# Performance work log

Measured on AMD Instinct MI355X. Metric: run time of the kernel, lower is better.

The kernel has to match this reference:

```python
import jax, jax.numpy as jnp
import numpy as np

N = 100000   # nodes
E = 1600000  # edges
F = 128      # num_features
H = 128      # embedding_size
C = 10       # num_classes
G = 64       # graphs in batch


def setup_inputs() -> dict:
    key = jax.random.key(0)
    ks = jax.random.split(key, 10)
    x = jax.random.normal(ks[0], (N, F), jnp.float32)
    edge_index = jax.random.randint(ks[1], (2, E), 0, N)
    batch_index = jnp.sort(jax.random.randint(ks[2], (N,), 0, G))
    glorot = lambda k, shape: jax.random.normal(k, shape, jnp.float32) / np.float32(np.sqrt(shape[0]))
    return {
        "x": x, "edge_index": edge_index, "batch_index": batch_index,
        "W0": glorot(ks[3], (F, H)), "b0": jnp.zeros((H,), jnp.float32),
        "W1": glorot(ks[4], (H, H)), "b1": jnp.zeros((H,), jnp.float32),
        "W2": glorot(ks[5], (H, H)), "b2": jnp.zeros((H,), jnp.float32),
        "W3": glorot(ks[6], (H, H)), "b3": jnp.zeros((H,), jnp.float32),
        "Wout": glorot(ks[7], (2 * H, C)), "bout": jnp.zeros((C,), jnp.float32),
    }


def gcn_conv(x, W, b, src, dst):
    """PyG GCNConv: self-loops + symmetric D^-1/2 (A+I) D^-1/2 normalization."""
    n = x.shape[0]
    # degree with self-loop: deg[i] = 1 + in-degree(i)
    deg = 1.0 + jax.ops.segment_sum(jnp.ones(dst.shape[0], x.dtype), dst, num_segments=n)
    dinv = jax.lax.rsqrt(deg)
    h = x @ W  # [N, H]
    norm = (dinv[src] * dinv[dst])[:, None]  # [E, 1]
    agg = jax.ops.segment_sum(h[src] * norm, dst, num_segments=n)  # scatter-add over edges
    agg = agg + h * (1.0 / deg)[:, None]  # self-loop contribution dinv[i]^2 * h[i]
    return agg + b


def reference(x, edge_index, batch_index, W0, b0, W1, b1, W2, b2, W3, b3, Wout, bout):
    src, dst = edge_index[0], edge_index[1]
    h = jnp.tanh(gcn_conv(x, W0, b0, src, dst))
    h = jnp.tanh(gcn_conv(h, W1, b1, src, dst))
    h = jnp.tanh(gcn_conv(h, W2, b2, src, dst))
    h = jnp.tanh(gcn_conv(h, W3, b3, src, dst))
    # global max pool + global mean pool over batch_index
    gmax = jax.ops.segment_max(h, batch_index, num_segments=G)
    cnt = jax.ops.segment_sum(jnp.ones((h.shape[0],), h.dtype), batch_index, num_segments=G)
    gmean = jax.ops.segment_sum(h, batch_index, num_segments=G) / jnp.maximum(cnt, 1.0)[:, None]
    pooled = jnp.concatenate([gmax, gmean], axis=1)  # [G, 2H]
    out = pooled @ Wout + bout  # [G, C]
    return out, pooled
```

## Files before the change

### kernel.cpp

```cpp
#include <hip/hip_runtime.h>
#include <hip/hip_fp16.h>
#include <cmath>

typedef __attribute__((ext_vector_type(8))) short short8;
typedef __attribute__((ext_vector_type(8))) unsigned short ushort8;
typedef __attribute__((ext_vector_type(8))) _Float16 f16x8;
typedef __attribute__((ext_vector_type(4))) float f32x4;

__device__ __forceinline__ unsigned pk_bf16(float a, float b) {
  unsigned r;
  asm("v_cvt_pk_bf16_f32 %0, %1, %2" : "=v"(r) : "v"(a), "v"(b));
  return r;
}

__device__ __forceinline__ float fast_tanh(float x) {
  float e2 = __expf(2.0f * x);
  return 1.0f - 2.0f * __builtin_amdgcn_rcpf(e2 + 1.0f);
}

#define FM_LO(A, U, W) \
  asm("v_fma_mix_f32 %0, %1, %2, %0 op_sel_hi:[1,0,0]" : "+v"(A) : "v"(U), "v"(W))
#define FM_HI(A, U, W) \
  asm("v_fma_mix_f32 %0, %1, %2, %0 op_sel:[1,0,0] op_sel_hi:[1,0,0]" : "+v"(A) : "v"(U), "v"(W))


__global__ __launch_bounds__(256) void count_wconv(
    const int* __restrict__ dst, int* __restrict__ cnt, int* __restrict__ epos,
    int E, int nc, const float* __restrict__ W0, const float* __restrict__ W1,
    const float* __restrict__ W2, const float* __restrict__ W3,
    unsigned short* __restrict__ Wt0Hi, unsigned short* __restrict__ Wt0Lo,
    unsigned short* __restrict__ WfHi, unsigned short* __restrict__ WfLo) {
  int b = blockIdx.x;
  if (b < nc) {
    int e = b * 256 + threadIdx.x;
    if (e < E) epos[e] = atomicAdd(&cnt[dst[e]], 1);
    return;
  }
  int t = (b - nc) * 256 + threadIdx.x;
  int l = t >> 13;
  int idx = t & 8191;
  const float* W = (l == 0) ? W0 : (l == 1) ? W1 : (l == 2) ? W2 : W3;
  int n = idx & 127, k = (idx >> 7) * 2;
  float w0 = W[k * 128 + n], w1 = W[(k + 1) * 128 + n];
  if (l == 0) {
    unsigned h01 = pk_bf16(w0, w1);
    float hf0 = __uint_as_float(h01 << 16);
    float hf1 = __uint_as_float(h01 & 0xFFFF0000u);
    unsigned l01 = pk_bf16(w0 - hf0, w1 - hf1);
    *(unsigned*)&Wt0Hi[n * 128 + k] = h01;
    *(unsigned*)&Wt0Lo[n * 128 + k] = l01;
  } else {
    __half2 hh = __float22half2_rn(make_float2(w0, w1));
    float r0 = __low2float(hh), r1 = __high2float(hh);
    __half2 ll = __float22half2_rn(make_float2((w0 - r0) * 1024.0f,
                                               (w1 - r1) * 1024.0f));
    *(__half2*)&WfHi[(l - 1) * 16384 + n * 128 + k] = hh;
    *(__half2*)&WfLo[(l - 1) * 16384 + n * 128 + k] = ll;
  }
}


__global__ __launch_bounds__(512) void scan_a(const int* __restrict__ cnt,
                                              int* __restrict__ rs,
                                              int* __restrict__ bsum,
                                              float* __restrict__ dinv,
                                              float* __restrict__ dinv2, int n) {
  __shared__ int s[512];
  int tid = threadIdx.x;
  int gid = blockIdx.x * 512 + tid;
  int v = (gid < n) ? cnt[gid] : 0;
  if (gid < n) {
    float deg = 1.0f + (float)v;
    dinv[gid] = rsqrtf(deg);
    dinv2[gid] = __builtin_amdgcn_rcpf(deg);
  }
  s[tid] = v;
  __syncthreads();
  for (int off = 1; off < 512; off <<= 1) {
    int t = (tid >= off) ? s[tid - off] : 0;
    __syncthreads();
    s[tid] += t;
    __syncthreads();
  }
  if (gid < n) rs[gid] = s[tid] - v;
  if (tid == 511) bsum[blockIdx.x] = s[511];
}

__global__ __launch_bounds__(256) void scan_b(const int* __restrict__ bsum,
                                              int* __restrict__ boff, int nb,
                                              const int* __restrict__ batch,
                                              int* __restrict__ gstart, int n,
                                              int G) {
  __shared__ int s[256];
  int tid = threadIdx.x;
  int v = (tid < nb) ? bsum[tid] : 0;
  s[tid] = v;
  __syncthreads();
  for (int off = 1; off < 256; off <<= 1) {
    int t = (tid >= off) ? s[tid - off] : 0;
    __syncthreads();
    s[tid] += t;
    __syncthreads();
  }
  if (tid < nb) boff[tid] = s[tid] - v;
  if (tid <= G) {
    int lo = 0, hi = n;
    while (lo < hi) {
      int mid = (lo + hi) >> 1;
      if (batch[mid] < tid) lo = mid + 1;
      else hi = mid;
    }
    gstart[tid] = lo;
  }
}

__global__ __launch_bounds__(512) void scan_c(const int* __restrict__ boff,
                                              int* __restrict__ rs, int n, int E) {
  int gid = blockIdx.x * 512 + threadIdx.x;
  if (gid < n) rs[gid] += boff[blockIdx.x];
  if (gid == 0) rs[n] = E;
}


__global__ __launch_bounds__(256) void fill_k(const int* __restrict__ src,
                                              const int* __restrict__ dst,
                                              const int* __restrict__ rs,
                                              const int* __restrict__ epos,
                                              const float* __restrict__ dinv,
                                              int2* __restrict__ edata, int E) {
  int e = blockIdx.x * 256 + threadIdx.x;
  if (e >= E) return;
  int s = src[e], d = dst[e];
  int pos = rs[d] + epos[e];
  int2 ed;
  ed.x = s;
  ed.y = __float_as_int(dinv[s] * dinv[d]);
  edata[pos] = ed;
}


#define LDK 136

__global__ __launch_bounds__(256) void gemm_mfma(const float* __restrict__ A,
                                                 const unsigned short* __restrict__ WtHi,
                                                 const unsigned short* __restrict__ WtLo,
                                                 __half* __restrict__ O, int M) {
  __shared__ unsigned short sHi[128 * LDK];
  __shared__ unsigned short sLo[128 * LDK];
  int tid = threadIdx.x;
#pragma unroll
  for (int i = 0; i < 8; ++i) {
    int c = tid + i * 256;
    int n = c >> 4;
    int off = (c & 15) * 8;
    *(ushort8*)&sHi[n * LDK + off] = *(const ushort8*)&WtHi[c * 8];
    *(ushort8*)&sLo[n * LDK + off] = *(const ushort8*)&WtLo[c * 8];
  }
  __syncthreads();

  int wv = tid >> 6, lane = tid & 63;
  int r0 = blockIdx.x * 128 + wv * 32;
  int lrow = lane & 15, lk = (lane >> 4) * 8;

  f32x4 acc[2][8] = {};
#pragma unroll
  for (int kk = 0; kk < 4; ++kk) {
    int k0 = kk * 32 + lk;
    short8 ahi[2], alo[2];
#pragma unroll
    for (int fr = 0; fr < 2; ++fr) {
      int row = r0 + fr * 16 + lrow;
      row = row < M ? row : M - 1;
      const float* ap = &A[(size_t)row * 128 + k0];
      float4 a0 = *(const float4*)ap;
      float4 a1 = *(const float4*)(ap + 4);
      union { short8 v; unsigned u32[4]; } h_, l_;
#define SPLIT2(slot, x, y)                              \
      {                                                 \
        unsigned hh = pk_bf16((x), (y));                \
        h_.u32[slot] = hh;                              \
        float hf0 = __uint_as_float(hh << 16);          \
        float hf1 = __uint_as_float(hh & 0xFFFF0000u);  \
        l_.u32[slot] = pk_bf16((x) - hf0, (y) - hf1);   \
      }
      SPLIT2(0, a0.x, a0.y)
      SPLIT2(1, a0.z, a0.w)
      SPLIT2(2, a1.x, a1.y)
      SPLIT2(3, a1.z, a1.w)
#undef SPLIT2
      ahi[fr] = h_.v;
      alo[fr] = l_.v;
    }
#pragma unroll
    for (int c = 0; c < 8; ++c) {
      int bidx = (c * 16 + lrow) * LDK + k0;
      short8 bhi = *(const short8*)&sHi[bidx];
      short8 blo = *(const short8*)&sLo[bidx];
#pragma unroll
      for (int fr = 0; fr < 2; ++fr) {
        acc[fr][c] = __builtin_amdgcn_mfma_f32_16x16x32_bf16(ahi[fr], bhi, acc[fr][c], 0, 0, 0);
        acc[fr][c] = __builtin_amdgcn_mfma_f32_16x16x32_bf16(ahi[fr], blo, acc[fr][c], 0, 0, 0);
        acc[fr][c] = __builtin_amdgcn_mfma_f32_16x16x32_bf16(alo[fr], bhi, acc[fr][c], 0, 0, 0);
      }
    }
  }
#pragma unroll
  for (int fr = 0; fr < 2; ++fr) {
#pragma unroll
    for (int c = 0; c < 8; ++c) {
#pragma unroll
      for (int r = 0; r < 4; ++r) {
        int row = r0 + fr * 16 + (lane >> 4) * 4 + r;
        if (row < M)
          O[(size_t)row * 128 + c * 16 + (lane & 15)] = __float2half(acc[fr][c][r]);
      }
    }
  }
}


__global__ __launch_bounds__(256) void gemm_f16(const __half* __restrict__ Hf,
                                                const unsigned short* __restrict__ Whi,
                                                const unsigned short* __restrict__ Wlo,
                                                __half* __restrict__ O, int M) {
  __shared__ unsigned short sHi[128 * LDK];
  __shared__ unsigned short sLo[128 * LDK];
  int tid = threadIdx.x;
#pragma unroll
  for (int i = 0; i < 8; ++i) {
    int c = tid + i * 256;
    int n = c >> 4;
    int off = (c & 15) * 8;
    *(ushort8*)&sHi[n * LDK + off] = *(const ushort8*)&Whi[c * 8];
    *(ushort8*)&sLo[n * LDK + off] = *(const ushort8*)&Wlo[c * 8];
  }
  __syncthreads();

  int wv = tid >> 6, lane = tid & 63;
  int r0 = blockIdx.x * 128 + wv * 32;
  int lrow = lane & 15, lk = (lane >> 4) * 8;

  f32x4 acc[2][8] = {};
  f32x4 accL[2][8] = {};
#pragma unroll
  for (int kk = 0; kk < 4; ++kk) {
    int k0 = kk * 32 + lk;
    f16x8 a[2];
#pragma unroll
    for (int fr = 0; fr < 2; ++fr) {
      int row = r0 + fr * 16 + lrow;
      row = row < M ? row : M - 1;
      a[fr] = *(const f16x8*)&Hf[(size_t)row * 128 + k0];
    }
#pragma unroll
    for (int c = 0; c < 8; ++c) {
      int bidx = (c * 16 + lrow) * LDK + k0;
      f16x8 bhi = *(const f16x8*)&sHi[bidx];
      f16x8 blo = *(const f16x8*)&sLo[bidx];
#pragma unroll
      for (int fr = 0; fr < 2; ++fr) {
        acc[fr][c] = __builtin_amdgcn_mfma_f32_16x16x32_f16(a[fr], bhi, acc[fr][c], 0, 0, 0);
        accL[fr][c] = __builtin_amdgcn_mfma_f32_16x16x32_f16(a[fr], blo, accL[fr][c], 0, 0, 0);
      }
    }
  }
  const float ls = 1.0f / 1024.0f;
#pragma unroll
  for (int fr = 0; fr < 2; ++fr) {
#pragma unroll
    for (int c = 0; c < 8; ++c) {
#pragma unroll
      for (int r = 0; r < 4; ++r) {
        int row = r0 + fr * 16 + (lane >> 4) * 4 + r;
        if (row < M)
          O[(size_t)row * 128 + c * 16 + (lane & 15)] =
              __float2half(acc[fr][c][r] + accL[fr][c][r] * ls);
      }
    }
  }
}


__global__ __launch_bounds__(256) void gather_k(const __half* __restrict__ h,
                                                const int* __restrict__ rs,
                                                const int2* __restrict__ edata,
                                                const float* __restrict__ dinv2,
                                                const float* __restrict__ bias,
                                                __half* __restrict__ Hf, int N) {
  int wid = (int)((blockIdx.x * (size_t)blockDim.x + threadIdx.x) >> 6);
  if (wid >= N) return;
  int lane = threadIdx.x & 63;
  int grp = lane >> 4;
  int li = lane & 15;
  int s = rs[wid], e = rs[wid + 1];
  const uint4* hrow = (const uint4*)h;
  const unsigned long long* ed64 = (const unsigned long long*)edata;

  float ac[8] = {};
  int niter = (e - s + 15) >> 4;
  int base = s + grp;
#define ACC(U, W)                                        \
  {                                                      \
    FM_LO(ac[0], (U).x, (W)); FM_HI(ac[1], (U).x, (W));  \
    FM_LO(ac[2], (U).y, (W)); FM_HI(ac[3], (U).y, (W));  \
    FM_LO(ac[4], (U).z, (W)); FM_HI(ac[5], (U).z, (W));  \
    FM_LO(ac[6], (U).w, (W)); FM_HI(ac[7], (U).w, (W));  \
  }
  for (int it = 0; it < niter; ++it, base += 16) {
    int p0 = base, p1 = base + 4, p2 = base + 8, p3 = base + 12;
    int c0 = p0 < e ? p0 : s, c1 = p1 < e ? p1 : s;
    int c2 = p2 < e ? p2 : s, c3 = p3 < e ? p3 : s;
    unsigned long long u0 = __builtin_nontemporal_load(&ed64[c0]);
    unsigned long long u1 = __builtin_nontemporal_load(&ed64[c1]);
    unsigned long long u2 = __builtin_nontemporal_load(&ed64[c2]);
    unsigned long long u3 = __builtin_nontemporal_load(&ed64[c3]);
    unsigned i0 = (unsigned)u0, i1 = (unsigned)u1;
    unsigned i2 = (unsigned)u2, i3 = (unsigned)u3;
    float w0 = p0 < e ? __uint_as_float((unsigned)(u0 >> 32)) : 0.0f;
    float w1 = p1 < e ? __uint_as_float((unsigned)(u1 >> 32)) : 0.0f;
    float w2 = p2 < e ? __uint_as_float((unsigned)(u2 >> 32)) : 0.0f;
    float w3 = p3 < e ? __uint_as_float((unsigned)(u3 >> 32)) : 0.0f;
    uint4 v0 = hrow[(size_t)i0 * 16 + li];
    uint4 v1 = hrow[(size_t)i1 * 16 + li];
    uint4 v2 = hrow[(size_t)i2 * 16 + li];
    uint4 v3 = hrow[(size_t)i3 * 16 + li];
    ACC(v0, w0) ACC(v1, w1) ACC(v2, w2) ACC(v3, w3)
  }
#undef ACC
#pragma unroll
  for (int j = 0; j < 8; ++j) {
    ac[j] += __shfl_xor(ac[j], 16);
    ac[j] += __shfl_xor(ac[j], 32);
  }

  float a0 = grp == 0 ? ac[0] : grp == 1 ? ac[2] : grp == 2 ? ac[4] : ac[6];
  float a1 = grp == 0 ? ac[1] : grp == 1 ? ac[3] : grp == 2 ? ac[5] : ac[7];

  float d2 = dinv2[wid];
  uint4 sv = hrow[(size_t)wid * 16 + li];
  unsigned su = grp == 0 ? sv.x : grp == 1 ? sv.y : grp == 2 ? sv.z : sv.w;
  float2 sj = __half22float2(*(__half2*)&su);
  float2 bj = *(const float2*)&bias[li * 8 + 2 * grp];
  float o0 = fast_tanh(a0 + sj.x * d2 + bj.x);
  float o1 = fast_tanh(a1 + sj.y * d2 + bj.y);

  __half2 hv = __float22half2_rn(make_float2(o0, o1));
  *(__half2*)&Hf[(size_t)wid * 128 + li * 8 + 2 * grp] = hv;
}


#define CH 16

__global__ __launch_bounds__(128) void pool_partial(const __half* __restrict__ Hf,
                                                    const int* __restrict__ gstart,
                                                    float* __restrict__ pmax,
                                                    float* __restrict__ psum) {
  int g = blockIdx.x, c = blockIdx.y, f = threadIdx.x;
  int s = gstart[g], e = gstart[g + 1];
  long long len = e - s;
  int cs = s + (int)(len * c / CH);
  int ce = s + (int)(len * (c + 1) / CH);
  float m = -INFINITY, sum = 0.f;
  for (int n = cs; n < ce; ++n) {
    float v = __half2float(Hf[(size_t)n * 128 + f]);
    m = fmaxf(m, v);
    sum += v;
  }
  pmax[((size_t)g * CH + c) * 128 + f] = m;
  psum[((size_t)g * CH + c) * 128 + f] = sum;
}

__global__ __launch_bounds__(128) void pool_head(const float* __restrict__ pmax,
                                                 const float* __restrict__ psum,
                                                 const int* __restrict__ gstart,
                                                 const float* __restrict__ Wout,
                                                 const float* __restrict__ bout,
                                                 float* __restrict__ out, int G) {
  __shared__ float pl[256];
  int g = blockIdx.x, f = threadIdx.x;
  float m = -INFINITY, s = 0.f;
  for (int c = 0; c < CH; ++c) {
    m = fmaxf(m, pmax[((size_t)g * CH + c) * 128 + f]);
    s += psum[((size_t)g * CH + c) * 128 + f];
  }
  int cnt = gstart[g + 1] - gstart[g];
  float mean = s / fmaxf((float)cnt, 1.0f);
  float* pooled = out + (size_t)G * 10;
  pooled[(size_t)g * 256 + f] = m;
  pooled[(size_t)g * 256 + 128 + f] = mean;
  pl[f] = m;
  pl[128 + f] = mean;
  __syncthreads();
  if (f < 10) {
    float acc = bout[f];
    for (int k = 0; k < 256; ++k) acc += pl[k] * Wout[k * 10 + f];
    out[(size_t)g * 10 + f] = acc;
  }
}


extern "C" void kernel_launch(void* const* d_in, const int* in_sizes, int n_in,
                              void* d_out, int out_size, void* d_ws, size_t ws_size,
                              hipStream_t stream) {
  const float* x = (const float*)d_in[0];
  const int* ei = (const int*)d_in[1];
  const int* batch = (const int*)d_in[2];
  const float* W[4] = {(const float*)d_in[3], (const float*)d_in[5],
                       (const float*)d_in[7], (const float*)d_in[9]};
  const float* Bz[4] = {(const float*)d_in[4], (const float*)d_in[6],
                        (const float*)d_in[8], (const float*)d_in[10]};
  const float* Wout = (const float*)d_in[11];
  const float* bout = (const float*)d_in[12];
  const int N = in_sizes[0] / 128;
  const int E = in_sizes[1] / 2;
  const int G = 64;
  const int* srcp = ei;
  const int* dstp = ei + E;
  float* out = (float*)d_out;

  char* wsb = (char*)d_ws;
  size_t off = 0;
  auto alloc = [&](size_t bytes) -> void* {
    void* p = wsb + off;
    off = (off + bytes + 255) & ~(size_t)255;
    return p;
  };
  __half* bufA = (__half*)alloc((size_t)N * 128 * 2);
  __half* Hf = (__half*)alloc((size_t)N * 128 * 2);
  size_t cnt_off = off;
  int* cnt = (int*)alloc((size_t)N * 4);
  size_t cnt_span = off - cnt_off;
  int* epos = (int*)alloc((size_t)E * 4);
  float* dinv = (float*)alloc((size_t)N * 4);
  float* dinv2 = (float*)alloc((size_t)N * 4);
  int* rs = (int*)alloc((size_t)(N + 1) * 4);
  int2* edata = (int2*)alloc((size_t)E * 8);
  int* bsum = (int*)alloc(4096);
  int* boff = (int*)alloc(4096);
  int* gstart = (int*)alloc(4096);
  float* pmax = (float*)alloc((size_t)G * CH * 128 * 4);
  float* psum = (float*)alloc((size_t)G * CH * 128 * 4);
  unsigned short* Wt0Hi = (unsigned short*)alloc(16384 * 2);
  unsigned short* Wt0Lo = (unsigned short*)alloc(16384 * 2);
  unsigned short* WfHi = (unsigned short*)alloc(3 * 16384 * 2);
  unsigned short* WfLo = (unsigned short*)alloc(3 * 16384 * 2);
  if (off > ws_size) return;

  hipMemsetAsync(wsb + cnt_off, 0, cnt_span, stream);

  int nc = (E + 255) / 256;
  count_wconv<<<nc + 128, 256, 0, stream>>>(dstp, cnt, epos, E, nc, W[0], W[1],
                                            W[2], W[3], Wt0Hi, Wt0Lo, WfHi, WfLo);
  int nsb = (N + 511) / 512;
  scan_a<<<nsb, 512, 0, stream>>>(cnt, rs, bsum, dinv, dinv2, N);
  scan_b<<<1, 256, 0, stream>>>(bsum, boff, nsb, batch, gstart, N, G);
  scan_c<<<nsb, 512, 0, stream>>>(boff, rs, N, E);
  fill_k<<<(E + 255) / 256, 256, 0, stream>>>(srcp, dstp, rs, epos, dinv, edata, E);

  int ggrid = (int)(((size_t)N * 64 + 255) / 256);
  for (int l = 0; l < 4; ++l) {
    if (l == 0)
      gemm_mfma<<<(N + 127) / 128, 256, 0, stream>>>(x, Wt0Hi, Wt0Lo, bufA, N);
    else
      gemm_f16<<<(N + 127) / 128, 256, 0, stream>>>(Hf, WfHi + (l - 1) * 16384,
                                                    WfLo + (l - 1) * 16384, bufA, N);
    gather_k<<<ggrid, 256, 0, stream>>>(bufA, rs, edata, dinv2, Bz[l], Hf, N);
  }

  pool_partial<<<dim3(G, CH), 128, 0, stream>>>(Hf, gstart, pmax, psum);
  pool_head<<<G, 128, 0, stream>>>(pmax, psum, gstart, Wout, bout, out, G);
}
```

Measured before the change: 516.3 us.

## Fuse layer-0 GEMM with edge counting and weight conversion in one interleaved launch

The first-layer GEMM, which does not depend on the graph structure, now runs in the same launch as the atomic in-degree counting and the fp16 weight conversion for layers 1-3. GEMM blocks are spread evenly among the other blocks so compute-bound MFMA work can overlap the atomic-bound counting. The layer-0 weight conversion moves into its own small kernel. The fused GEMM also drops its LDS staging of the weights and reads the bf16 hi/lo weights directly from global memory, which may add memory traffic and lose the padded layout that avoided LDS bank conflicts.

```diff
diff --git a/kernel.cpp b/kernel.cpp
--- a/kernel.cpp
+++ b/kernel.cpp
@@ -24,142 +24,29 @@
   asm("v_fma_mix_f32 %0, %1, %2, %0 op_sel:[1,0,0] op_sel_hi:[1,0,0]" : "+v"(A) : "v"(U), "v"(W))
 
 
-__global__ __launch_bounds__(256) void count_wconv(
-    const int* __restrict__ dst, int* __restrict__ cnt, int* __restrict__ epos,
-    int E, int nc, const float* __restrict__ W0, const float* __restrict__ W1,
-    const float* __restrict__ W2, const float* __restrict__ W3,
-    unsigned short* __restrict__ Wt0Hi, unsigned short* __restrict__ Wt0Lo,
-    unsigned short* __restrict__ WfHi, unsigned short* __restrict__ WfLo) {
-  int b = blockIdx.x;
-  if (b < nc) {
-    int e = b * 256 + threadIdx.x;
-    if (e < E) epos[e] = atomicAdd(&cnt[dst[e]], 1);
-    return;
-  }
-  int t = (b - nc) * 256 + threadIdx.x;
-  int l = t >> 13;
-  int idx = t & 8191;
-  const float* W = (l == 0) ? W0 : (l == 1) ? W1 : (l == 2) ? W2 : W3;
+__global__ __launch_bounds__(256) void wconv0(const float* __restrict__ W0,
+                                              unsigned short* __restrict__ Wt0Hi,
+                                              unsigned short* __restrict__ Wt0Lo) {
+  int idx = blockIdx.x * 256 + threadIdx.x;
+  if (idx >= 8192) return;
   int n = idx & 127, k = (idx >> 7) * 2;
-  float w0 = W[k * 128 + n], w1 = W[(k + 1) * 128 + n];
-  if (l == 0) {
-    unsigned h01 = pk_bf16(w0, w1);
-    float hf0 = __uint_as_float(h01 << 16);
-    float hf1 = __uint_as_float(h01 & 0xFFFF0000u);
-    unsigned l01 = pk_bf16(w0 - hf0, w1 - hf1);
-    *(unsigned*)&Wt0Hi[n * 128 + k] = h01;
-    *(unsigned*)&Wt0Lo[n * 128 + k] = l01;
-  } else {
-    __half2 hh = __float22half2_rn(make_float2(w0, w1));
-    float r0 = __low2float(hh), r1 = __high2float(hh);
-    __half2 ll = __float22half2_rn(make_float2((w0 - r0) * 1024.0f,
-                                               (w1 - r1) * 1024.0f));
-    *(__half2*)&WfHi[(l - 1) * 16384 + n * 128 + k] = hh;
-    *(__half2*)&WfLo[(l - 1) * 16384 + n * 128 + k] = ll;
-  }
-}
-
-
-__global__ __launch_bounds__(512) void scan_a(const int* __restrict__ cnt,
-                                              int* __restrict__ rs,
-                                              int* __restrict__ bsum,
-                                              float* __restrict__ dinv,
-                                              float* __restrict__ dinv2, int n) {
-  __shared__ int s[512];
+  float w0 = W0[k * 128 + n], w1 = W0[(k + 1) * 128 + n];
+  unsigned h01 = pk_bf16(w0, w1);
+  float hf0 = __uint_as_float(h01 << 16);
+  float hf1 = __uint_as_float(h01 & 0xFFFF0000u);
+  unsigned l01 = pk_bf16(w0 - hf0, w1 - hf1);
+  *(unsigned*)&Wt0Hi[n * 128 + k] = h01;
+  *(unsigned*)&Wt0Lo[n * 128 + k] = l01;
+}
+
+
+__device__ __forceinline__ void gemm0_block(int bx, const float* __restrict__ A,
+                                            const unsigned short* __restrict__ WtHi,
+                                            const unsigned short* __restrict__ WtLo,
+                                            __half* __restrict__ O, int M) {
   int tid = threadIdx.x;
-  int gid = blockIdx.x * 512 + tid;
-  int v = (gid < n) ? cnt[gid] : 0;
-  if (gid < n) {
-    float deg = 1.0f + (float)v;
-    dinv[gid] = rsqrtf(deg);
-    dinv2[gid] = __builtin_amdgcn_rcpf(deg);
-  }
-  s[tid] = v;
-  __syncthreads();
-  for (int off = 1; off < 512; off <<= 1) {
-    int t = (tid >= off) ? s[tid - off] : 0;
-    __syncthreads();
-    s[tid] += t;
-    __syncthreads();
-  }
-  if (gid < n) rs[gid] = s[tid] - v;
-  if (tid == 511) bsum[blockIdx.x] = s[511];
-}
-
-__global__ __launch_bounds__(256) void scan_b(const int* __restrict__ bsum,
-                                              int* __restrict__ boff, int nb,
-                                              const int* __restrict__ batch,
-                                              int* __restrict__ gstart, int n,
-                                              int G) {
-  __shared__ int s[256];
-  int tid = threadIdx.x;
-  int v = (tid < nb) ? bsum[tid] : 0;
-  s[tid] = v;
-  __syncthreads();
-  for (int off = 1; off < 256; off <<= 1) {
-    int t = (tid >= off) ? s[tid - off] : 0;
-    __syncthreads();
-    s[tid] += t;
-    __syncthreads();
-  }
-  if (tid < nb) boff[tid] = s[tid] - v;
-  if (tid <= G) {
-    int lo = 0, hi = n;
-    while (lo < hi) {
-      int mid = (lo + hi) >> 1;
-      if (batch[mid] < tid) lo = mid + 1;
-      else hi = mid;
-    }
-    gstart[tid] = lo;
-  }
-}
-
-__global__ __launch_bounds__(512) void scan_c(const int* __restrict__ boff,
-                                              int* __restrict__ rs, int n, int E) {
-  int gid = blockIdx.x * 512 + threadIdx.x;
-  if (gid < n) rs[gid] += boff[blockIdx.x];
-  if (gid == 0) rs[n] = E;
-}
-
-
-__global__ __launch_bounds__(256) void fill_k(const int* __restrict__ src,
-                                              const int* __restrict__ dst,
-                                              const int* __restrict__ rs,
-                                              const int* __restrict__ epos,
-                                              const float* __restrict__ dinv,
-                                              int2* __restrict__ edata, int E) {
-  int e = blockIdx.x * 256 + threadIdx.x;
-  if (e >= E) return;
-  int s = src[e], d = dst[e];
-  int pos = rs[d] + epos[e];
-  int2 ed;
-  ed.x = s;
-  ed.y = __float_as_int(dinv[s] * dinv[d]);
-  edata[pos] = ed;
-}
-
-
-#define LDK 136
-
-__global__ __launch_bounds__(256) void gemm_mfma(const float* __restrict__ A,
-                                                 const unsigned short* __restrict__ WtHi,
-                                                 const unsigned short* __restrict__ WtLo,
-                                                 __half* __restrict__ O, int M) {
-  __shared__ unsigned short sHi[128 * LDK];
-  __shared__ unsigned short sLo[128 * LDK];
-  int tid = threadIdx.x;
-#pragma unroll
-  for (int i = 0; i < 8; ++i) {
-    int c = tid + i * 256;
-    int n = c >> 4;
-    int off = (c & 15) * 8;
-    *(ushort8*)&sHi[n * LDK + off] = *(const ushort8*)&WtHi[c * 8];
-    *(ushort8*)&sLo[n * LDK + off] = *(const ushort8*)&WtLo[c * 8];
-  }
-  __syncthreads();
-
   int wv = tid >> 6, lane = tid & 63;
-  int r0 = blockIdx.x * 128 + wv * 32;
+  int r0 = bx * 128 + wv * 32;
   int lrow = lane & 15, lk = (lane >> 4) * 8;
 
   f32x4 acc[2][8] = {};
@@ -193,9 +80,9 @@
     }
 #pragma unroll
     for (int c = 0; c < 8; ++c) {
-      int bidx = (c * 16 + lrow) * LDK + k0;
-      short8 bhi = *(const short8*)&sHi[bidx];
-      short8 blo = *(const short8*)&sLo[bidx];
+      int bidx = (c * 16 + lrow) * 128 + k0;
+      short8 bhi = *(const short8*)&WtHi[bidx];
+      short8 blo = *(const short8*)&WtLo[bidx];
 #pragma unroll
       for (int fr = 0; fr < 2; ++fr) {
         acc[fr][c] = __builtin_amdgcn_mfma_f32_16x16x32_bf16(ahi[fr], bhi, acc[fr][c], 0, 0, 0);
@@ -218,6 +105,123 @@
   }
 }
 
+
+__global__ __launch_bounds__(256) void mega_a(
+    const int* __restrict__ dst, int* __restrict__ cnt, int* __restrict__ epos,
+    int E, int ncnt, int ngemm, int p,
+    const float* __restrict__ W1, const float* __restrict__ W2,
+    const float* __restrict__ W3, unsigned short* __restrict__ WfHi,
+    unsigned short* __restrict__ WfLo,
+    const float* __restrict__ x, const unsigned short* __restrict__ Wt0Hi,
+    const unsigned short* __restrict__ Wt0Lo, __half* __restrict__ bufA, int M) {
+  int bid = blockIdx.x;
+  int g = bid / p;
+  if ((bid % p) == 0 && g < ngemm) {
+    gemm0_block(g, x, Wt0Hi, Wt0Lo, bufA, M);
+    return;
+  }
+  int before = (g < ngemm) ? (g + 1) : ngemm;
+  int other = bid - before;
+  if (other < ncnt) {
+    int e = other * 256 + threadIdx.x;
+    if (e < E) epos[e] = atomicAdd(&cnt[dst[e]], 1);
+    return;
+  }
+  int t = (other - ncnt) * 256 + threadIdx.x;
+  int l = 1 + (t >> 13);
+  int idx = t & 8191;
+  const float* W = (l == 1) ? W1 : (l == 2) ? W2 : W3;
+  int n = idx & 127, k = (idx >> 7) * 2;
+  float w0 = W[k * 128 + n], w1 = W[(k + 1) * 128 + n];
+  __half2 hh = __float22half2_rn(make_float2(w0, w1));
+  float r0 = __low2float(hh), r1 = __high2float(hh);
+  __half2 ll = __float22half2_rn(make_float2((w0 - r0) * 1024.0f,
+                                             (w1 - r1) * 1024.0f));
+  *(__half2*)&WfHi[(l - 1) * 16384 + n * 128 + k] = hh;
+  *(__half2*)&WfLo[(l - 1) * 16384 + n * 128 + k] = ll;
+}
+
+
+__global__ __launch_bounds__(512) void scan_a(const int* __restrict__ cnt,
+                                              int* __restrict__ rs,
+                                              int* __restrict__ bsum,
+                                              float* __restrict__ dinv,
+                                              float* __restrict__ dinv2, int n) {
+  __shared__ int s[512];
+  int tid = threadIdx.x;
+  int gid = blockIdx.x * 512 + tid;
+  int v = (gid < n) ? cnt[gid] : 0;
+  if (gid < n) {
+    float deg = 1.0f + (float)v;
+    dinv[gid] = rsqrtf(deg);
+    dinv2[gid] = __builtin_amdgcn_rcpf(deg);
+  }
+  s[tid] = v;
+  __syncthreads();
+  for (int off = 1; off < 512; off <<= 1) {
+    int t = (tid >= off) ? s[tid - off] : 0;
+    __syncthreads();
+    s[tid] += t;
+    __syncthreads();
+  }
+  if (gid < n) rs[gid] = s[tid] - v;
+  if (tid == 511) bsum[blockIdx.x] = s[511];
+}
+
+__global__ __launch_bounds__(256) void scan_b(const int* __restrict__ bsum,
+                                              int* __restrict__ boff, int nb,
+                                              const int* __restrict__ batch,
+                                              int* __restrict__ gstart, int n,
+                                              int G) {
+  __shared__ int s[256];
+  int tid = threadIdx.x;
+  int v = (tid < nb) ? bsum[tid] : 0;
+  s[tid] = v;
+  __syncthreads();
+  for (int off = 1; off < 256; off <<= 1) {
+    int t = (tid >= off) ? s[tid - off] : 0;
+    __syncthreads();
+    s[tid] += t;
+    __syncthreads();
+  }
+  if (tid < nb) boff[tid] = s[tid] - v;
+  if (tid <= G) {
+    int lo = 0, hi = n;
+    while (lo < hi) {
+      int mid = (lo + hi) >> 1;
+      if (batch[mid] < tid) lo = mid + 1;
+      else hi = mid;
+    }
+    gstart[tid] = lo;
+  }
+}
+
+__global__ __launch_bounds__(512) void scan_c(const int* __restrict__ boff,
+                                              int* __restrict__ rs, int n, int E) {
+  int gid = blockIdx.x * 512 + threadIdx.x;
+  if (gid < n) rs[gid] += boff[blockIdx.x];
+  if (gid == 0) rs[n] = E;
+}
+
+
+__global__ __launch_bounds__(256) void fill_k(const int* __restrict__ src,
+                                              const int* __restrict__ dst,
+                                              const int* __restrict__ rs,
+                                              const int* __restrict__ epos,
+                                              const float* __restrict__ dinv,
+                                              int2* __restrict__ edata, int E) {
+  int e = blockIdx.x * 256 + threadIdx.x;
+  if (e >= E) return;
+  int s = src[e], d = dst[e];
+  int pos = rs[d] + epos[e];
+  int2 ed;
+  ed.x = s;
+  ed.y = __float_as_int(dinv[s] * dinv[d]);
+  edata[pos] = ed;
+}
+
+
+#define LDK 136
 
 __global__ __launch_bounds__(256) void gemm_f16(const __half* __restrict__ Hf,
                                                 const unsigned short* __restrict__ Whi,
@@ -448,9 +452,16 @@
 
   hipMemsetAsync(wsb + cnt_off, 0, cnt_span, stream);
 
-  int nc = (E + 255) / 256;
-  count_wconv<<<nc + 128, 256, 0, stream>>>(dstp, cnt, epos, E, nc, W[0], W[1],
-                                            W[2], W[3], Wt0Hi, Wt0Lo, WfHi, WfLo);
+  wconv0<<<32, 256, 0, stream>>>(W[0], Wt0Hi, Wt0Lo);
+
+  int ncnt = (E + 255) / 256;
+  int ngemm = (N + 127) / 128;
+  int total = ncnt + 96 + ngemm;
+  int p = total / ngemm;
+  mega_a<<<total, 256, 0, stream>>>(dstp, cnt, epos, E, ncnt, ngemm, p, W[1],
+                                    W[2], W[3], WfHi, WfLo, x, Wt0Hi, Wt0Lo,
+                                    bufA, N);
+
   int nsb = (N + 511) / 512;
   scan_a<<<nsb, 512, 0, stream>>>(cnt, rs, bsum, dinv, dinv2, N);
   scan_b<<<1, 256, 0, stream>>>(bsum, boff, nsb, batch, gstart, N, G);
@@ -459,9 +470,7 @@
 
   int ggrid = (int)(((size_t)N * 64 + 255) / 256);
   for (int l = 0; l < 4; ++l) {
-    if (l == 0)
-      gemm_mfma<<<(N + 127) / 128, 256, 0, stream>>>(x, Wt0Hi, Wt0Lo, bufA, N);
-    else
+    if (l > 0)
       gemm_f16<<<(N + 127) / 128, 256, 0, stream>>>(Hf, WfHi + (l - 1) * 16384,
                                                     WfLo + (l - 1) * 16384, bufA, N);
     gather_k<<<ggrid, 256, 0, stream>>>(bufA, rs, edata, dinv2, Bz[l], Hf, N);
```

Result: no change. 515.9 us (-0.1%).
